# Optimization experiments

Hardware: AMD Instinct MI355X
Metric: run time of the kernel (lower is better)

## Reference

```python
import jax, jax.numpy as jnp
import numpy as np

D, NH, B, N, P = 512, 4, 4096, 30, 30  # embed_dim, num_heads, batch, seq, num_positional_embeddings


def _ln(x, g, b, eps=1e-5):
    mu = jnp.mean(x, axis=-1, keepdims=True)
    var = jnp.mean((x - mu) ** 2, axis=-1, keepdims=True)
    return g * (x - mu) / jnp.sqrt(var + eps) + b


def setup_inputs() -> dict:
    key = jax.random.key(0)
    ks = jax.random.split(key, 8)
    s = 0.02
    x = jax.random.normal(ks[0], (B, N, D), jnp.float32)
    attention_mask = jnp.zeros((B, N), dtype=bool)
    order = jax.random.randint(ks[1], (B, N), 0, P)
    num_docs = jnp.full((B,), float(N), jnp.float32)
    docs_weights = jax.random.uniform(ks[2], (B, N), jnp.float32)
    clusters_centroids = jax.random.normal(ks[3], (B, D), jnp.float32)
    pos_emb = (jax.random.normal(ks[4], (P + 1, D), jnp.float32) * s).at[P].set(0.0)
    fc1_w1 = jax.random.normal(ks[5], (2 * D + 1, D), jnp.float32) * s
    fc1_b1 = jnp.zeros((D,), jnp.float32)
    fc1_w2 = jax.random.normal(ks[6], (D, NH), jnp.float32) * s
    fc1_b2 = jnp.zeros((NH,), jnp.float32)
    fc2_w = jax.random.normal(ks[7], (NH * D, D), jnp.float32) * s
    fc2_b = jnp.zeros((D,), jnp.float32)
    return dict(
        x=x, attention_mask=attention_mask, order=order, num_docs=num_docs,
        docs_weights=docs_weights, clusters_centroids=clusters_centroids,
        pos_emb=pos_emb, fc1_w1=fc1_w1, fc1_b1=fc1_b1, fc1_w2=fc1_w2, fc1_b2=fc1_b2,
        fc2_w=fc2_w, fc2_b=fc2_b,
        ln1_g=jnp.ones((D,), jnp.float32), ln1_b=jnp.zeros((D,), jnp.float32),
        ln2_g=jnp.ones((NH * D,), jnp.float32), ln2_b=jnp.zeros((NH * D,), jnp.float32),
        ln3_g=jnp.ones((D,), jnp.float32), ln3_b=jnp.zeros((D,), jnp.float32),
        ln4_g=jnp.ones((D,), jnp.float32), ln4_b=jnp.zeros((D,), jnp.float32),
    )


def reference(x, attention_mask, order, num_docs, docs_weights, clusters_centroids,
              pos_emb, fc1_w1, fc1_b1, fc1_w2, fc1_b2, fc2_w, fc2_b,
              ln1_g, ln1_b, ln2_g, ln2_b, ln3_g, ln3_b, ln4_g, ln4_b):
    eps = 1e-8
    # norm_1: F.normalize(x, dim=2, eps=1e-8)
    xn = x / jnp.maximum(jnp.linalg.norm(x, axis=2, keepdims=True), eps)
    # input layernorm
    x1 = _ln(xn, ln1_g, ln1_b)
    xp = x1 + pos_emb[order]  # [B,N,D]
    # weighted mean pool of x_positions
    mp = jnp.sum(xp * docs_weights[:, :, None], axis=1, keepdims=True) / num_docs[:, None, None]  # [B,1,D]
    # cosine similarity between mean_pool and each token (torch eps=1e-8)
    num = jnp.sum(mp * xp, axis=2)  # [B,N]
    den = jnp.maximum(jnp.linalg.norm(mp, axis=2) * jnp.linalg.norm(xp, axis=2), eps)
    cos = (num / den)[:, :, None]  # [B,N,1]
    fc1_in = jnp.concatenate([xp, jnp.broadcast_to(mp, xp.shape), cos], axis=2)  # [B,N,2D+1]
    Z = jnp.tanh(fc1_in @ fc1_w1 + fc1_b1) @ fc1_w2 + fc1_b2  # [B,N,H]
    Z = jnp.where(attention_mask[:, :, None], -jnp.inf, Z)
    A = jax.nn.softmax(Z, axis=1)  # [B,N,H]
    b, n, h = A.shape
    d = x1.shape[2]
    # Faithful to the original reshape([B*H, N, 1]) on a [B,N,H]-contiguous tensor
    A_h = A.reshape(b, h, n)
    Hh = jnp.einsum('bhn,bnd->bhd', A_h, x1).reshape(b, h * d)  # [B, H*D]
    # residual: weighted mean pool of x (post ln1), tiled per head
    mpx = jnp.sum(x1 * docs_weights[:, :, None], axis=1) / num_docs[:, None]  # [B,D]
    Hh = _ln(Hh + jnp.tile(mpx, (1, h)), ln2_g, ln2_b)
    pred = _ln(Hh @ fc2_w + fc2_b, ln3_g, ln3_b)  # afterFC layernorm
    pred = _ln(pred + jnp.mean(Hh.reshape(b, h, d), axis=1), ln4_g, ln4_b)
    return pred
```

## Files before the change

### kernel.cpp

```cpp
#include <hip/hip_runtime.h>
#include <hip/hip_bf16.h>

#define B_ 4096
#define N_ 30
#define D_ 512
#define H_ 4
#define M_ (B_*N_)
#define PE_ROWS 31

typedef unsigned short u16;
typedef __attribute__((ext_vector_type(8))) short bf16x8;
typedef __attribute__((ext_vector_type(4))) float f32x4;

__device__ __forceinline__ float bf2f(u16 s) { return __uint_as_float(((unsigned)s) << 16); }
__device__ __forceinline__ u16 f2bf(float f) {
  __hip_bfloat16 h = __float2bfloat16(f);
  return *reinterpret_cast<u16*>(&h);
}

__device__ __forceinline__ float ftanh(float x) {
  float e = __expf(2.f * x);
  return 1.f - 2.f * __builtin_amdgcn_rcpf(e + 1.f);
}

__device__ __forceinline__ void gll16(const void* g, void* l) {
  __builtin_amdgcn_global_load_lds(
      (const __attribute__((address_space(1))) unsigned int*)g,
      (__attribute__((address_space(3))) unsigned int*)l, 16, 0, 0);
}

__device__ __forceinline__ float wsum(float v) {
  #pragma unroll
  for (int m = 32; m >= 1; m >>= 1) v += __shfl_xor(v, m);
  return v;
}
__device__ __forceinline__ float wmax(float v) {
  #pragma unroll
  for (int m = 32; m >= 1; m >>= 1) v = fmaxf(v, __shfl_xor(v, m));
  return v;
}

__global__ __launch_bounds__(512) void k1_prep(
    const float* __restrict__ x, const int* __restrict__ order,
    const float* __restrict__ ndocs, const float* __restrict__ dw,
    const float* __restrict__ pe, const float* __restrict__ g1,
    const float* __restrict__ bln1,
    u16* __restrict__ x1bf, u16* __restrict__ mpbf, float* __restrict__ mpx,
    float* __restrict__ cosb) {
  __shared__ float lds_mp[8*512];
  __shared__ float lds_mpx[8*512];
  __shared__ float xps[32];
  int b = blockIdx.x;
  int tid = threadIdx.x;
  int wid = tid >> 6, lane = tid & 63;
  int d0 = lane * 8;
  float g[8], bl[8];
  *(float4*)&g[0]  = *(const float4*)&g1[d0];
  *(float4*)&g[4]  = *(const float4*)&g1[d0+4];
  *(float4*)&bl[0] = *(const float4*)&bln1[d0];
  *(float4*)&bl[4] = *(const float4*)&bln1[d0+4];
  float xp_reg[4][8];
  float accmp[8] = {0,0,0,0,0,0,0,0}, accmpx[8] = {0,0,0,0,0,0,0,0};
  #pragma unroll
  for (int t = 0; t < 4; ++t) {
    int n = wid + 8*t;
    if (n < N_) {
      int tok = b*N_ + n;
      float v[8];
      *(float4*)&v[0] = *(const float4*)&x[(size_t)tok*D_ + d0];
      *(float4*)&v[4] = *(const float4*)&x[(size_t)tok*D_ + d0 + 4];
      float ss = 0.f, sm = 0.f;
      #pragma unroll
      for (int i = 0; i < 8; ++i) { ss += v[i]*v[i]; sm += v[i]; }
      ss = wsum(ss); sm = wsum(sm);
      float inv = 1.f / fmaxf(sqrtf(ss), 1e-8f);
      float mu = sm * inv * (1.f/D_);
      float m2 = ss*inv*inv*(1.f/D_);
      float rs = 1.f / sqrtf(m2 - mu*mu + 1e-5f);
      int o = order[tok];
      float p8[8];
      *(float4*)&p8[0] = *(const float4*)&pe[(size_t)o*D_ + d0];
      *(float4*)&p8[4] = *(const float4*)&pe[(size_t)o*D_ + d0 + 4];
      float wv = dw[tok];
      float sq = 0.f;
      bf16x8 xb;
      #pragma unroll
      for (int i = 0; i < 8; ++i) {
        float x1v = g[i]*((v[i]*inv - mu)*rs) + bl[i];
        xb[i] = (short)f2bf(x1v);
        float xpv = x1v + p8[i];
        xp_reg[t][i] = xpv;
        accmp[i]  += wv*xpv;
        accmpx[i] += wv*x1v;
        sq += xpv*xpv;
      }
      *(bf16x8*)&x1bf[(size_t)tok*D_ + d0] = xb;
      sq = wsum(sq);
      if (lane == 0) xps[n] = sq;
    }
  }
  #pragma unroll
  for (int i = 0; i < 8; i += 4) {
    *(float4*)&lds_mp[wid*512 + d0 + i]  = *(float4*)&accmp[i];
    *(float4*)&lds_mpx[wid*512 + d0 + i] = *(float4*)&accmpx[i];
  }
  __syncthreads();
  float invnd = 1.f / ndocs[b];
  float mpv[8] = {0,0,0,0,0,0,0,0}, mpxv[8] = {0,0,0,0,0,0,0,0};
  #pragma unroll
  for (int w = 0; w < 8; ++w) {
    #pragma unroll
    for (int i = 0; i < 8; i += 4) {
      float4 a = *(float4*)&lds_mp[w*512 + d0 + i];
      mpv[i+0] += a.x; mpv[i+1] += a.y; mpv[i+2] += a.z; mpv[i+3] += a.w;
      float4 c = *(float4*)&lds_mpx[w*512 + d0 + i];
      mpxv[i+0] += c.x; mpxv[i+1] += c.y; mpxv[i+2] += c.z; mpxv[i+3] += c.w;
    }
  }
  #pragma unroll
  for (int i = 0; i < 8; ++i) { mpv[i] *= invnd; mpxv[i] *= invnd; }
  if (wid == 0) {
    bf16x8 mb;
    #pragma unroll
    for (int i = 0; i < 8; ++i) mb[i] = (short)f2bf(mpv[i]);
    *(bf16x8*)&mpbf[(size_t)b*D_ + d0] = mb;
  }
  if (wid == 1) {
    #pragma unroll
    for (int i = 0; i < 8; i += 4)
      *(float4*)&mpx[(size_t)b*D_ + d0 + i] = *(float4*)&mpxv[i];
  }
  float mn = 0.f;
  #pragma unroll
  for (int i = 0; i < 8; ++i) mn += mpv[i]*mpv[i];
  float mpn = sqrtf(wsum(mn));
  #pragma unroll
  for (int t = 0; t < 4; ++t) {
    int n = wid + 8*t;
    if (n < N_) {
      float dot = 0.f;
      #pragma unroll
      for (int i = 0; i < 8; ++i) dot += mpv[i]*xp_reg[t][i];
      dot = wsum(dot);
      if (lane == 0)
        cosb[b*N_ + n] = dot / fmaxf(mpn * sqrtf(xps[n]), 1e-8f);
    }
  }
}

__global__ __launch_bounds__(512) void k_pew(
    const float* __restrict__ pe, const float* __restrict__ w1,
    float* __restrict__ peW) {
  int p = blockIdx.x, j = threadIdx.x;
  float acc = 0.f;
  for (int dd = 0; dd < D_; ++dd) acc += pe[p*D_ + dd] * w1[(size_t)dd*D_ + j];
  peW[p*D_ + j] = acc;
}

__global__ __launch_bounds__(256) void k_tcvt(
    const float* __restrict__ in, u16* __restrict__ out, int Kdim, int Jdim) {
  __shared__ float tile[64][65];
  int k0 = blockIdx.x * 64, j0 = blockIdx.y * 64;
  int t = threadIdx.x;
  int tr = t >> 4, tc4 = (t & 15) * 4;
  #pragma unroll
  for (int i = 0; i < 4; ++i) {
    int k = k0 + tr + i*16;
    float4 v = *(const float4*)&in[(size_t)k*Jdim + j0 + tc4];
    tile[tr + i*16][tc4+0] = v.x;
    tile[tr + i*16][tc4+1] = v.y;
    tile[tr + i*16][tc4+2] = v.z;
    tile[tr + i*16][tc4+3] = v.w;
  }
  __syncthreads();
  #pragma unroll
  for (int i = 0; i < 4; ++i) {
    int j = tr + i*16;
    uint2 u;
    u.x = (unsigned)f2bf(tile[tc4+0][j]) | ((unsigned)f2bf(tile[tc4+1][j]) << 16);
    u.y = (unsigned)f2bf(tile[tc4+2][j]) | ((unsigned)f2bf(tile[tc4+3][j]) << 16);
    *(uint2*)&out[(size_t)(j0+j)*Kdim + k0 + tc4] = u;
  }
}

__global__ __launch_bounds__(256, 3) void k2_mpw(
    const u16* __restrict__ mpbf, const u16* __restrict__ w1mT,
    const float* __restrict__ b1, float* __restrict__ mpW) {
  __shared__ __align__(16) u16 As[128*64];
  __shared__ __align__(16) u16 Bs[128*64];
  int tid = threadIdx.x;
  int lane = tid & 63, wid = tid >> 6;
  int wg = (blockIdx.x & 7)*16 + (blockIdx.x >> 3);
  int colb = wg & 3, rowb = wg >> 2;
  int row0 = rowb*128, col0 = colb*128;
  int wm = wid >> 1, wn = wid & 1;
  int lr = lane & 15, lk = lane >> 4;
  int srow = lane >> 3;
  int skel = ((lane & 7) ^ srow) << 3;
  f32x4 acc[4][4];
  #pragma unroll
  for (int nf = 0; nf < 4; ++nf) {
    float bv = b1[col0 + wn*64 + nf*16 + lr];
    #pragma unroll
    for (int mf = 0; mf < 4; ++mf)
      acc[mf][nf] = (f32x4){bv, bv, bv, bv};
  }
  for (int k0 = 0; k0 < D_; k0 += 64) {
    __syncthreads();
    #pragma unroll
    for (int i = 0; i < 4; ++i) {
      int rb = wid*32 + i*8;
      gll16(&mpbf[(size_t)(row0 + rb + srow)*D_ + k0 + skel], &As[rb*64]);
      gll16(&w1mT[(size_t)(col0 + rb + srow)*D_ + k0 + skel], &Bs[rb*64]);
    }
    __syncthreads();
    #pragma unroll
    for (int kk = 0; kk < 2; ++kk) {
      int kb = (kk*64 + lk*16) ^ ((lr & 7) << 4);
      bf16x8 a[4];
      #pragma unroll
      for (int mf = 0; mf < 4; ++mf)
        a[mf] = *(const bf16x8*)((const char*)As + (wm*64 + mf*16 + lr)*128 + kb);
      #pragma unroll
      for (int nf = 0; nf < 4; ++nf) {
        bf16x8 bfr = *(const bf16x8*)((const char*)Bs + (wn*64 + nf*16 + lr)*128 + kb);
        #pragma unroll
        for (int mf = 0; mf < 4; ++mf)
          acc[mf][nf] = __builtin_amdgcn_mfma_f32_16x16x32_bf16(a[mf], bfr, acc[mf][nf], 0, 0, 0);
      }
    }
  }
  #pragma unroll
  for (int mf = 0; mf < 4; ++mf)
    #pragma unroll
    for (int nf = 0; nf < 4; ++nf)
      #pragma unroll
      for (int r = 0; r < 4; ++r) {
        int m = row0 + wm*64 + mf*16 + lk*4 + r;
        int j = col0 + wn*64 + nf*16 + lr;
        mpW[(size_t)m*D_ + j] = acc[mf][nf][r];
      }
}

__global__ __launch_bounds__(256, 3) void k4_fc1(
    const u16* __restrict__ x1bf, const u16* __restrict__ w1T,
    const float* __restrict__ w1, const float* __restrict__ w2,
    const int* __restrict__ order, const float* __restrict__ cosb,
    const float* __restrict__ mpW, const float* __restrict__ peW,
    float* __restrict__ Zp) {
  __shared__ __align__(16) u16 As[128*64];
  __shared__ __align__(16) u16 Bs[128*64];
  __shared__ float zred[2*128*4];
  int tid = threadIdx.x;
  int lane = tid & 63, wid = tid >> 6;
  int col0 = blockIdx.x * 128;
  int row0 = blockIdx.y * 128;
  int wm = wid >> 1, wn = wid & 1;
  int lr = lane & 15, lk = lane >> 4;
  int srow = lane >> 3;
  int skel = ((lane & 7) ^ srow) << 3;
  float wl[4];
  #pragma unroll
  for (int nf = 0; nf < 4; ++nf)
    wl[nf] = w1[(size_t)1024*D_ + col0 + wn*64 + nf*16 + lr];
  f32x4 acc[4][4];
  #pragma unroll
  for (int mf = 0; mf < 4; ++mf) {
    #pragma unroll
    for (int r = 0; r < 4; ++r) {
      int m = row0 + wm*64 + mf*16 + lk*4 + r;
      int bidx = m / N_;
      int o = order[m];
      float cs = cosb[m];
      #pragma unroll
      for (int nf = 0; nf < 4; ++nf) {
        int jl = col0 + wn*64 + nf*16 + lr;
        acc[mf][nf][r] = mpW[(size_t)bidx*D_ + jl] + peW[o*D_ + jl] + cs*wl[nf];
      }
    }
  }
  for (int k0 = 0; k0 < D_; k0 += 64) {
    __syncthreads();
    #pragma unroll
    for (int i = 0; i < 4; ++i) {
      int rb = wid*32 + i*8;
      gll16(&x1bf[(size_t)(row0 + rb + srow)*D_ + k0 + skel], &As[rb*64]);
      gll16(&w1T [(size_t)(col0 + rb + srow)*D_ + k0 + skel], &Bs[rb*64]);
    }
    __syncthreads();
    #pragma unroll
    for (int kk = 0; kk < 2; ++kk) {
      int kb = (kk*64 + lk*16) ^ ((lr & 7) << 4);
      bf16x8 a[4];
      #pragma unroll
      for (int mf = 0; mf < 4; ++mf)
        a[mf] = *(const bf16x8*)((const char*)As + (wm*64 + mf*16 + lr)*128 + kb);
      #pragma unroll
      for (int nf = 0; nf < 4; ++nf) {
        bf16x8 bfr = *(const bf16x8*)((const char*)Bs + (wn*64 + nf*16 + lr)*128 + kb);
        #pragma unroll
        for (int mf = 0; mf < 4; ++mf)
          acc[mf][nf] = __builtin_amdgcn_mfma_f32_16x16x32_bf16(a[mf], bfr, acc[mf][nf], 0, 0, 0);
      }
    }
  }
  float w2r[4][4];
  #pragma unroll
  for (int nf = 0; nf < 4; ++nf)
    *(float4*)w2r[nf] = *(const float4*)&w2[(col0 + wn*64 + nf*16 + lr)*4];
  #pragma unroll
  for (int mf = 0; mf < 4; ++mf) {
    #pragma unroll
    for (int r = 0; r < 4; ++r) {
      int rowt = wm*64 + mf*16 + lk*4 + r;
      float z0=0.f, z1=0.f, z2=0.f, z3=0.f;
      #pragma unroll
      for (int nf = 0; nf < 4; ++nf) {
        float t = ftanh(acc[mf][nf][r]);
        z0 += t * w2r[nf][0]; z1 += t * w2r[nf][1];
        z2 += t * w2r[nf][2]; z3 += t * w2r[nf][3];
      }
      #pragma unroll
      for (int msk = 1; msk <= 8; msk <<= 1) {
        z0 += __shfl_xor(z0, msk); z1 += __shfl_xor(z1, msk);
        z2 += __shfl_xor(z2, msk); z3 += __shfl_xor(z3, msk);
      }
      if (lr == 0)
        *(float4*)&zred[(wn*128 + rowt)*4] = make_float4(z0, z1, z2, z3);
    }
  }
  __syncthreads();
  if (tid < 128) {
    float4 s0 = *(float4*)&zred[tid*4];
    float4 s1 = *(float4*)&zred[(128 + tid)*4];
    *(float4*)&Zp[((size_t)blockIdx.x*M_ + row0 + tid)*4] =
        make_float4(s0.x+s1.x, s0.y+s1.y, s0.z+s1.z, s0.w+s1.w);
  }
}

__global__ __launch_bounds__(512) void k5_attn(
    const float* __restrict__ Zp, const float* __restrict__ b2,
    const unsigned char* __restrict__ amask, const u16* __restrict__ x1bf,
    const float* __restrict__ mpx, const float* __restrict__ g2,
    const float* __restrict__ bln2, u16* __restrict__ Hh2bf,
    float* __restrict__ hmean) {
  __shared__ float abuf[8][120];
  int tid = threadIdx.x;
  int wid = tid >> 6, lane = tid & 63;
  int b = blockIdx.x*8 + wid;
  bool act = lane < N_;
  int tok = b*N_ + (act ? lane : 0);
  float zz[4] = {-INFINITY, -INFINITY, -INFINITY, -INFINITY};
  if (act) {
    float4 za = *(const float4*)&Zp[(size_t)tok*4];
    float4 zb = *(const float4*)&Zp[((size_t)M_ + tok)*4];
    float4 zc = *(const float4*)&Zp[((size_t)2*M_ + tok)*4];
    float4 zd = *(const float4*)&Zp[((size_t)3*M_ + tok)*4];
    float4 bv = *(const float4*)b2;
    zz[0] = za.x+zb.x+zc.x+zd.x+bv.x; zz[1] = za.y+zb.y+zc.y+zd.y+bv.y;
    zz[2] = za.z+zb.z+zc.z+zd.z+bv.z; zz[3] = za.w+zb.w+zc.w+zd.w+bv.w;
    if (amask[tok]) { zz[0]=zz[1]=zz[2]=zz[3]=-INFINITY; }
  }
  float p[4];
  #pragma unroll
  for (int h = 0; h < 4; ++h) {
    float mx = wmax(zz[h]);
    float e = act ? __expf(zz[h] - mx) : 0.f;
    float s = wsum(e);
    p[h] = e / s;
  }
  if (act) *(float4*)&abuf[wid][lane*4] = make_float4(p[0], p[1], p[2], p[3]);
  __syncthreads();
  float hv[4][8] = {};
  const u16* xr = &x1bf[(size_t)b*N_*D_ + lane*8];
  for (int j = 0; j < N_; ++j) {
    bf16x8 xb = *(const bf16x8*)(xr + (size_t)j*D_);
    float xv[8];
    #pragma unroll
    for (int e = 0; e < 8; ++e) xv[e] = bf2f((u16)xb[e]);
    #pragma unroll
    for (int i = 0; i < 4; ++i) {
      float a = abuf[wid][i*N_ + j];
      #pragma unroll
      for (int e = 0; e < 8; ++e) hv[i][e] += a * xv[e];
    }
  }
  float mpxv[8];
  *(float4*)&mpxv[0] = *(const float4*)&mpx[(size_t)b*D_ + lane*8];
  *(float4*)&mpxv[4] = *(const float4*)&mpx[(size_t)b*D_ + lane*8 + 4];
  float s1 = 0.f, s2 = 0.f;
  #pragma unroll
  for (int i = 0; i < 4; ++i)
    #pragma unroll
    for (int e = 0; e < 8; ++e) {
      hv[i][e] += mpxv[e];
      s1 += hv[i][e];
      s2 += hv[i][e]*hv[i][e];
    }
  s1 = wsum(s1); s2 = wsum(s2);
  float mu = s1 * (1.f/2048.f);
  float var = s2 * (1.f/2048.f) - mu*mu;
  float rs = 1.f / sqrtf(var + 1e-5f);
  float hm[8] = {0,0,0,0,0,0,0,0};
  #pragma unroll
  for (int i = 0; i < 4; ++i) {
    int idx = i*D_ + lane*8;
    float gg[8], bb[8];
    *(float4*)&gg[0] = *(const float4*)&g2[idx];
    *(float4*)&gg[4] = *(const float4*)&g2[idx+4];
    *(float4*)&bb[0] = *(const float4*)&bln2[idx];
    *(float4*)&bb[4] = *(const float4*)&bln2[idx+4];
    bf16x8 ob;
    #pragma unroll
    for (int e = 0; e < 8; ++e) {
      float v = gg[e]*((hv[i][e]-mu)*rs) + bb[e];
      hm[e] += v;
      ob[e] = (short)f2bf(v);
    }
    *(bf16x8*)&Hh2bf[(size_t)b*2048 + idx] = ob;
  }
  #pragma unroll
  for (int e = 0; e < 8; ++e) hm[e] *= 0.25f;
  *(float4*)&hmean[(size_t)b*D_ + lane*8]     = *(float4*)&hm[0];
  *(float4*)&hmean[(size_t)b*D_ + lane*8 + 4] = *(float4*)&hm[4];
}

__global__ __launch_bounds__(256, 3) void k6_fc2(
    const u16* __restrict__ Hh2bf, const u16* __restrict__ fwT,
    float* __restrict__ pred_p) {
  __shared__ __align__(16) u16 As[128*64];
  __shared__ __align__(16) u16 Bs[128*64];
  int tid = threadIdx.x;
  int lane = tid & 63, wid = tid >> 6;
  int wg = (blockIdx.x & 7)*64 + (blockIdx.x >> 3);
  int kz = wg >> 7;
  int rem = wg & 127;
  int rowb = rem >> 2, colb = rem & 3;
  int row0 = rowb*128, col0 = colb*128;
  int kbase = kz*512;
  int wm = wid >> 1, wn = wid & 1;
  int lr = lane & 15, lk = lane >> 4;
  int srow = lane >> 3;
  int skel = ((lane & 7) ^ srow) << 3;
  f32x4 acc[4][4] = {};
  for (int k0 = kbase; k0 < kbase + 512; k0 += 64) {
    __syncthreads();
    #pragma unroll
    for (int i = 0; i < 4; ++i) {
      int rb = wid*32 + i*8;
      gll16(&Hh2bf[(size_t)(row0 + rb + srow)*2048 + k0 + skel], &As[rb*64]);
      gll16(&fwT  [(size_t)(col0 + rb + srow)*2048 + k0 + skel], &Bs[rb*64]);
    }
    __syncthreads();
    #pragma unroll
    for (int kk = 0; kk < 2; ++kk) {
      int kb = (kk*64 + lk*16) ^ ((lr & 7) << 4);
      bf16x8 a[4];
      #pragma unroll
      for (int mf = 0; mf < 4; ++mf)
        a[mf] = *(const bf16x8*)((const char*)As + (wm*64 + mf*16 + lr)*128 + kb);
      #pragma unroll
      for (int nf = 0; nf < 4; ++nf) {
        bf16x8 bfr = *(const bf16x8*)((const char*)Bs + (wn*64 + nf*16 + lr)*128 + kb);
        #pragma unroll
        for (int mf = 0; mf < 4; ++mf)
          acc[mf][nf] = __builtin_amdgcn_mfma_f32_16x16x32_bf16(a[mf], bfr, acc[mf][nf], 0, 0, 0);
      }
    }
  }
  float* dst = pred_p + (size_t)kz * B_ * D_;
  #pragma unroll
  for (int mf = 0; mf < 4; ++mf)
    #pragma unroll
    for (int nf = 0; nf < 4; ++nf)
      #pragma unroll
      for (int r = 0; r < 4; ++r) {
        int m = row0 + wm*64 + mf*16 + lk*4 + r;
        int j = col0 + wn*64 + nf*16 + lr;
        dst[(size_t)m*D_ + j] = acc[mf][nf][r];
      }
}

__global__ __launch_bounds__(512) void k7_final(
    const float* __restrict__ pred_p, const float* __restrict__ hmean,
    const float* __restrict__ fb,
    const float* __restrict__ g3, const float* __restrict__ b3,
    const float* __restrict__ g4, const float* __restrict__ b4,
    float* __restrict__ out) {
  int tid = threadIdx.x;
  int wid = tid >> 6, lane = tid & 63;
  int b = blockIdx.x*8 + wid;
  int d0 = lane*8;
  size_t i = (size_t)b*D_ + d0;
  size_t BD = (size_t)B_*D_;
  float p[8];
  #pragma unroll
  for (int e = 0; e < 8; e += 4) {
    float4 a0 = *(const float4*)&pred_p[i+e];
    float4 a1 = *(const float4*)&pred_p[BD+i+e];
    float4 a2 = *(const float4*)&pred_p[2*BD+i+e];
    float4 a3 = *(const float4*)&pred_p[3*BD+i+e];
    float4 fv = *(const float4*)&fb[d0+e];
    p[e+0] = a0.x+a1.x+a2.x+a3.x+fv.x;
    p[e+1] = a0.y+a1.y+a2.y+a3.y+fv.y;
    p[e+2] = a0.z+a1.z+a2.z+a3.z+fv.z;
    p[e+3] = a0.w+a1.w+a2.w+a3.w+fv.w;
  }
  float s1 = 0.f, s2 = 0.f;
  #pragma unroll
  for (int e = 0; e < 8; ++e) { s1 += p[e]; s2 += p[e]*p[e]; }
  s1 = wsum(s1); s2 = wsum(s2);
  float mu = s1*(1.f/D_);
  float var = s2*(1.f/D_) - mu*mu;
  float rs = 1.f / sqrtf(var + 1e-5f);
  float g3v[8], b3v[8], hmv[8], q[8];
  *(float4*)&g3v[0] = *(const float4*)&g3[d0];
  *(float4*)&g3v[4] = *(const float4*)&g3[d0+4];
  *(float4*)&b3v[0] = *(const float4*)&b3[d0];
  *(float4*)&b3v[4] = *(const float4*)&b3[d0+4];
  *(float4*)&hmv[0] = *(const float4*)&hmean[i];
  *(float4*)&hmv[4] = *(const float4*)&hmean[i+4];
  float t1 = 0.f, t2 = 0.f;
  #pragma unroll
  for (int e = 0; e < 8; ++e) {
    q[e] = g3v[e]*((p[e]-mu)*rs) + b3v[e] + hmv[e];
    t1 += q[e]; t2 += q[e]*q[e];
  }
  t1 = wsum(t1); t2 = wsum(t2);
  mu = t1*(1.f/D_);
  var = t2*(1.f/D_) - mu*mu;
  rs = 1.f / sqrtf(var + 1e-5f);
  float g4v[8], b4v[8], o[8];
  *(float4*)&g4v[0] = *(const float4*)&g4[d0];
  *(float4*)&g4v[4] = *(const float4*)&g4[d0+4];
  *(float4*)&b4v[0] = *(const float4*)&b4[d0];
  *(float4*)&b4v[4] = *(const float4*)&b4[d0+4];
  #pragma unroll
  for (int e = 0; e < 8; ++e) o[e] = g4v[e]*((q[e]-mu)*rs) + b4v[e];
  *(float4*)&out[i]   = *(float4*)&o[0];
  *(float4*)&out[i+4] = *(float4*)&o[4];
}

extern "C" void kernel_launch(void* const* d_in, const int* in_sizes, int n_in,
                              void* d_out, int out_size, void* d_ws, size_t ws_size,
                              hipStream_t stream) {
  const float* x      = (const float*)d_in[0];
  const unsigned char* amask = (const unsigned char*)d_in[1];
  const int*   order  = (const int*)d_in[2];
  const float* ndocs  = (const float*)d_in[3];
  const float* dw     = (const float*)d_in[4];
  const float* pe     = (const float*)d_in[6];
  const float* w1     = (const float*)d_in[7];
  const float* b1     = (const float*)d_in[8];
  const float* w2     = (const float*)d_in[9];
  const float* b2     = (const float*)d_in[10];
  const float* fw     = (const float*)d_in[11];
  const float* fb     = (const float*)d_in[12];
  const float* g1     = (const float*)d_in[13];
  const float* bln1   = (const float*)d_in[14];
  const float* g2     = (const float*)d_in[15];
  const float* bln2   = (const float*)d_in[16];
  const float* g3     = (const float*)d_in[17];
  const float* b3     = (const float*)d_in[18];
  const float* g4     = (const float*)d_in[19];
  const float* b4     = (const float*)d_in[20];
  float* out = (float*)d_out;

  char* ws = (char*)d_ws;
  size_t off = 0;
  u16*   x1bf   = (u16*)(ws + off);   off += (size_t)M_*D_*2;
  u16*   mpbf   = (u16*)(ws + off);   off += (size_t)B_*D_*2;
  float* mpx    = (float*)(ws + off); off += (size_t)B_*D_*4;
  float* mpW    = (float*)(ws + off); off += (size_t)B_*D_*4;
  float* hmean  = (float*)(ws + off); off += (size_t)B_*D_*4;
  float* peW    = (float*)(ws + off); off += (size_t)PE_ROWS*D_*4;
  float* cosb   = (float*)(ws + off); off += (size_t)M_*4;
  float* Zp     = (float*)(ws + off); off += (size_t)4*M_*4*4;
  float* pred_p = (float*)(ws + off); off += (size_t)4*B_*D_*4;
  u16*   Hh2bf  = (u16*)(ws + off);   off += (size_t)B_*2048*2;
  u16*   w1T    = (u16*)(ws + off);   off += (size_t)D_*D_*2;
  u16*   w1mT   = (u16*)(ws + off);   off += (size_t)D_*D_*2;
  u16*   fwT    = (u16*)(ws + off);   off += (size_t)D_*2048*2;
  (void)ws_size; (void)in_sizes; (void)n_in; (void)out_size;

  k_tcvt<<<dim3(8, 8), 256, 0, stream>>>(w1, w1T, 512, 512);
  k_tcvt<<<dim3(8, 8), 256, 0, stream>>>(w1 + 512*512, w1mT, 512, 512);
  k_tcvt<<<dim3(32, 8), 256, 0, stream>>>(fw, fwT, 2048, 512);
  k_pew<<<PE_ROWS, 512, 0, stream>>>(pe, w1, peW);
  k1_prep<<<B_, 512, 0, stream>>>(x, order, ndocs, dw, pe, g1, bln1,
                                  x1bf, mpbf, mpx, cosb);
  k2_mpw<<<128, 256, 0, stream>>>(mpbf, w1mT, b1, mpW);
  k4_fc1<<<dim3(4, M_/128), 256, 0, stream>>>(x1bf, w1T, w1, w2, order, cosb,
                                              mpW, peW, Zp);
  k5_attn<<<B_/8, 512, 0, stream>>>(Zp, b2, amask, x1bf, mpx, g2, bln2,
                                    Hh2bf, hmean);
  k6_fc2<<<512, 256, 0, stream>>>(Hh2bf, fwT, pred_p);
  k7_final<<<B_/8, 512, 0, stream>>>(pred_p, hmean, fb, g3, b3, g4, b4, out);
}
```

Baseline: 325.9 us.

## Enlarge fc1 GEMM tiles to 256x256 with double-buffered LDS and block swizzle

The fc1 kernel moves from 128x128 tiles with 256 threads to 256x256 tiles with 512 threads. Each wave now holds an 8x4 grid of MFMA accumulators. Global-to-LDS loads are double-buffered so the next K slice is fetched while the current one is computed, which leaves one barrier per iteration. Block indices are swizzled, and the Z partial sums now come from two column blocks instead of four, so the attention kernel reads half as many partials. The cost is a large LDS footprint (128 KB, so likely one block per CU) and heavy register pressure, which risks spills or low occupancy.

```diff
diff --git a/kernel.cpp b/kernel.cpp
--- a/kernel.cpp
+++ b/kernel.cpp
@@ -242,20 +242,19 @@
       }
 }
 
-__global__ __launch_bounds__(256, 3) void k4_fc1(
+__global__ __launch_bounds__(512, 2) void k4_fc1(
     const u16* __restrict__ x1bf, const u16* __restrict__ w1T,
     const float* __restrict__ w1, const float* __restrict__ w2,
     const int* __restrict__ order, const float* __restrict__ cosb,
     const float* __restrict__ mpW, const float* __restrict__ peW,
     float* __restrict__ Zp) {
-  __shared__ __align__(16) u16 As[128*64];
-  __shared__ __align__(16) u16 Bs[128*64];
-  __shared__ float zred[2*128*4];
+  __shared__ __align__(16) u16 buf[2][2*256*64];
   int tid = threadIdx.x;
   int lane = tid & 63, wid = tid >> 6;
-  int col0 = blockIdx.x * 128;
-  int row0 = blockIdx.y * 128;
-  int wm = wid >> 1, wn = wid & 1;
+  int wg = (blockIdx.x & 7)*120 + (blockIdx.x >> 3);
+  int colb = wg & 1, rowb = wg >> 1;
+  int col0 = colb*256, row0 = rowb*256;
+  int wm = wid >> 2, wn = wid & 3;
   int lr = lane & 15, lk = lane >> 4;
   int srow = lane >> 3;
   int skel = ((lane & 7) ^ srow) << 3;
@@ -263,12 +262,12 @@
   #pragma unroll
   for (int nf = 0; nf < 4; ++nf)
     wl[nf] = w1[(size_t)1024*D_ + col0 + wn*64 + nf*16 + lr];
-  f32x4 acc[4][4];
-  #pragma unroll
-  for (int mf = 0; mf < 4; ++mf) {
+  f32x4 acc[8][4];
+  #pragma unroll
+  for (int mf = 0; mf < 8; ++mf) {
     #pragma unroll
     for (int r = 0; r < 4; ++r) {
-      int m = row0 + wm*64 + mf*16 + lk*4 + r;
+      int m = row0 + wm*128 + mf*16 + lk*4 + r;
       int bidx = m / N_;
       int o = order[m];
       float cs = cosb[m];
@@ -279,40 +278,55 @@
       }
     }
   }
-  for (int k0 = 0; k0 < D_; k0 += 64) {
-    __syncthreads();
-    #pragma unroll
-    for (int i = 0; i < 4; ++i) {
-      int rb = wid*32 + i*8;
-      gll16(&x1bf[(size_t)(row0 + rb + srow)*D_ + k0 + skel], &As[rb*64]);
-      gll16(&w1T [(size_t)(col0 + rb + srow)*D_ + k0 + skel], &Bs[rb*64]);
-    }
-    __syncthreads();
+  float w2r[4][4];
+  #pragma unroll
+  for (int nf = 0; nf < 4; ++nf)
+    *(float4*)w2r[nf] = *(const float4*)&w2[(col0 + wn*64 + nf*16 + lr)*4];
+
+#define K4_STAGE(c, k0)                                                     \
+  {                                                                         \
+    u16* Ad = &buf[c][0];                                                   \
+    u16* Bd = &buf[c][16384];                                               \
+    _Pragma("unroll")                                                       \
+    for (int i = 0; i < 4; ++i) {                                           \
+      int rb = wid*32 + i*8;                                                \
+      gll16(&x1bf[(size_t)(row0 + rb + srow)*D_ + (k0) + skel], &Ad[rb*64]);\
+      gll16(&w1T [(size_t)(col0 + rb + srow)*D_ + (k0) + skel], &Bd[rb*64]);\
+    }                                                                       \
+  }
+
+  K4_STAGE(0, 0);
+  __syncthreads();
+  int cur = 0;
+  for (int t = 0; t < 8; ++t) {
+    if (t < 7) K4_STAGE(cur^1, (t+1)*64);
+    const u16* A = &buf[cur][0];
+    const u16* Bx = &buf[cur][16384];
     #pragma unroll
     for (int kk = 0; kk < 2; ++kk) {
       int kb = (kk*64 + lk*16) ^ ((lr & 7) << 4);
-      bf16x8 a[4];
-      #pragma unroll
-      for (int mf = 0; mf < 4; ++mf)
-        a[mf] = *(const bf16x8*)((const char*)As + (wm*64 + mf*16 + lr)*128 + kb);
+      bf16x8 a[8];
+      #pragma unroll
+      for (int mf = 0; mf < 8; ++mf)
+        a[mf] = *(const bf16x8*)((const char*)A + (wm*128 + mf*16 + lr)*128 + kb);
       #pragma unroll
       for (int nf = 0; nf < 4; ++nf) {
-        bf16x8 bfr = *(const bf16x8*)((const char*)Bs + (wn*64 + nf*16 + lr)*128 + kb);
+        bf16x8 bfr = *(const bf16x8*)((const char*)Bx + (wn*64 + nf*16 + lr)*128 + kb);
         #pragma unroll
-        for (int mf = 0; mf < 4; ++mf)
+        for (int mf = 0; mf < 8; ++mf)
           acc[mf][nf] = __builtin_amdgcn_mfma_f32_16x16x32_bf16(a[mf], bfr, acc[mf][nf], 0, 0, 0);
       }
     }
-  }
-  float w2r[4][4];
-  #pragma unroll
-  for (int nf = 0; nf < 4; ++nf)
-    *(float4*)w2r[nf] = *(const float4*)&w2[(col0 + wn*64 + nf*16 + lr)*4];
-  #pragma unroll
-  for (int mf = 0; mf < 4; ++mf) {
+    __syncthreads();
+    cur ^= 1;
+  }
+#undef K4_STAGE
+  float* zred = (float*)buf;
+  #pragma unroll
+  for (int mf = 0; mf < 8; ++mf) {
     #pragma unroll
     for (int r = 0; r < 4; ++r) {
-      int rowt = wm*64 + mf*16 + lk*4 + r;
+      int rowt = wm*128 + mf*16 + lk*4 + r;
       float z0=0.f, z1=0.f, z2=0.f, z3=0.f;
       #pragma unroll
       for (int nf = 0; nf < 4; ++nf) {
@@ -326,15 +340,18 @@
         z2 += __shfl_xor(z2, msk); z3 += __shfl_xor(z3, msk);
       }
       if (lr == 0)
-        *(float4*)&zred[(wn*128 + rowt)*4] = make_float4(z0, z1, z2, z3);
+        *(float4*)&zred[(wn*256 + rowt)*4] = make_float4(z0, z1, z2, z3);
     }
   }
   __syncthreads();
-  if (tid < 128) {
+  if (tid < 256) {
     float4 s0 = *(float4*)&zred[tid*4];
-    float4 s1 = *(float4*)&zred[(128 + tid)*4];
-    *(float4*)&Zp[((size_t)blockIdx.x*M_ + row0 + tid)*4] =
-        make_float4(s0.x+s1.x, s0.y+s1.y, s0.z+s1.z, s0.w+s1.w);
+    float4 s1 = *(float4*)&zred[(256 + tid)*4];
+    float4 s2 = *(float4*)&zred[(512 + tid)*4];
+    float4 s3 = *(float4*)&zred[(768 + tid)*4];
+    *(float4*)&Zp[((size_t)colb*M_ + row0 + tid)*4] =
+        make_float4(s0.x+s1.x+s2.x+s3.x, s0.y+s1.y+s2.y+s3.y,
+                    s0.z+s1.z+s2.z+s3.z, s0.w+s1.w+s2.w+s3.w);
   }
 }
 
@@ -354,11 +371,9 @@
   if (act) {
     float4 za = *(const float4*)&Zp[(size_t)tok*4];
     float4 zb = *(const float4*)&Zp[((size_t)M_ + tok)*4];
-    float4 zc = *(const float4*)&Zp[((size_t)2*M_ + tok)*4];
-    float4 zd = *(const float4*)&Zp[((size_t)3*M_ + tok)*4];
     float4 bv = *(const float4*)b2;
-    zz[0] = za.x+zb.x+zc.x+zd.x+bv.x; zz[1] = za.y+zb.y+zc.y+zd.y+bv.y;
-    zz[2] = za.z+zb.z+zc.z+zd.z+bv.z; zz[3] = za.w+zb.w+zc.w+zd.w+bv.w;
+    zz[0] = za.x+zb.x+bv.x; zz[1] = za.y+zb.y+bv.y;
+    zz[2] = za.z+zb.z+bv.z; zz[3] = za.w+zb.w+bv.w;
     if (amask[tok]) { zz[0]=zz[1]=zz[2]=zz[3]=-INFINITY; }
   }
   float p[4];
@@ -575,7 +590,7 @@
   float* hmean  = (float*)(ws + off); off += (size_t)B_*D_*4;
   float* peW    = (float*)(ws + off); off += (size_t)PE_ROWS*D_*4;
   float* cosb   = (float*)(ws + off); off += (size_t)M_*4;
-  float* Zp     = (float*)(ws + off); off += (size_t)4*M_*4*4;
+  float* Zp     = (float*)(ws + off); off += (size_t)2*M_*4*4;
   float* pred_p = (float*)(ws + off); off += (size_t)4*B_*D_*4;
   u16*   Hh2bf  = (u16*)(ws + off);   off += (size_t)B_*2048*2;
   u16*   w1T    = (u16*)(ws + off);   off += (size_t)D_*D_*2;
@@ -590,8 +605,8 @@
   k1_prep<<<B_, 512, 0, stream>>>(x, order, ndocs, dw, pe, g1, bln1,
                                   x1bf, mpbf, mpx, cosb);
   k2_mpw<<<128, 256, 0, stream>>>(mpbf, w1mT, b1, mpW);
-  k4_fc1<<<dim3(4, M_/128), 256, 0, stream>>>(x1bf, w1T, w1, w2, order, cosb,
-                                              mpW, peW, Zp);
+  k4_fc1<<<960, 512, 0, stream>>>(x1bf, w1T, w1, w2, order, cosb,
+                                  mpW, peW, Zp);
   k5_attn<<<B_/8, 512, 0, stream>>>(Zp, b2, amask, x1bf, mpx, g2, bln2,
                                     Hh2bf, hmean);
   k6_fc2<<<512, 256, 0, stream>>>(Hh2bf, fwT, pred_p);
```

Result: slower. 403.3 us (+23.8%).

## Compute full 512-wide fc1 row tile per block, dropping partial Z buffers

Applied to the files above, without the earlier changes.

The fc1 kernel now uses 512-thread blocks that each cover 128 rows across all 512 output columns, so the A tile is loaded once rather than four times and the tanh·w2 reduction completes inside the block. Z is written directly, with no four-way partial buffer for the attention kernel to sum. Block indices are swizzled across 8 groups, and zred reuses the As shared memory. In exchange, each thread keeps twice the accumulators (128 floats), which raises register pressure, and the Bs tile grows to 64KB, which limits occupancy.

```diff
diff --git a/kernel.cpp b/kernel.cpp
--- a/kernel.cpp
+++ b/kernel.cpp
@@ -242,28 +242,27 @@
       }
 }
 
-__global__ __launch_bounds__(256, 3) void k4_fc1(
+__global__ __launch_bounds__(512, 2) void k4_fc1(
     const u16* __restrict__ x1bf, const u16* __restrict__ w1T,
     const float* __restrict__ w1, const float* __restrict__ w2,
     const int* __restrict__ order, const float* __restrict__ cosb,
     const float* __restrict__ mpW, const float* __restrict__ peW,
-    float* __restrict__ Zp) {
+    float* __restrict__ Z) {
   __shared__ __align__(16) u16 As[128*64];
-  __shared__ __align__(16) u16 Bs[128*64];
-  __shared__ float zred[2*128*4];
+  __shared__ __align__(16) u16 Bs[512*64];
   int tid = threadIdx.x;
   int lane = tid & 63, wid = tid >> 6;
-  int col0 = blockIdx.x * 128;
-  int row0 = blockIdx.y * 128;
-  int wm = wid >> 1, wn = wid & 1;
+  int wg = (blockIdx.x & 7)*120 + (blockIdx.x >> 3);
+  int row0 = wg * 128;
+  int wm = wid >> 2, wn = wid & 3;
   int lr = lane & 15, lk = lane >> 4;
   int srow = lane >> 3;
   int skel = ((lane & 7) ^ srow) << 3;
-  float wl[4];
-  #pragma unroll
-  for (int nf = 0; nf < 4; ++nf)
-    wl[nf] = w1[(size_t)1024*D_ + col0 + wn*64 + nf*16 + lr];
-  f32x4 acc[4][4];
+  float wl[8];
+  #pragma unroll
+  for (int nf = 0; nf < 8; ++nf)
+    wl[nf] = w1[(size_t)1024*D_ + wn*128 + nf*16 + lr];
+  f32x4 acc[4][8];
   #pragma unroll
   for (int mf = 0; mf < 4; ++mf) {
     #pragma unroll
@@ -273,8 +272,8 @@
       int o = order[m];
       float cs = cosb[m];
       #pragma unroll
-      for (int nf = 0; nf < 4; ++nf) {
-        int jl = col0 + wn*64 + nf*16 + lr;
+      for (int nf = 0; nf < 8; ++nf) {
+        int jl = wn*128 + nf*16 + lr;
         acc[mf][nf][r] = mpW[(size_t)bidx*D_ + jl] + peW[o*D_ + jl] + cs*wl[nf];
       }
     }
@@ -282,10 +281,14 @@
   for (int k0 = 0; k0 < D_; k0 += 64) {
     __syncthreads();
     #pragma unroll
-    for (int i = 0; i < 4; ++i) {
-      int rb = wid*32 + i*8;
+    for (int i = 0; i < 2; ++i) {
+      int rb = wid*16 + i*8;
       gll16(&x1bf[(size_t)(row0 + rb + srow)*D_ + k0 + skel], &As[rb*64]);
-      gll16(&w1T [(size_t)(col0 + rb + srow)*D_ + k0 + skel], &Bs[rb*64]);
+    }
+    #pragma unroll
+    for (int i = 0; i < 8; ++i) {
+      int rb = wid*64 + i*8;
+      gll16(&w1T[(size_t)(rb + srow)*D_ + k0 + skel], &Bs[rb*64]);
     }
     __syncthreads();
     #pragma unroll
@@ -296,18 +299,20 @@
       for (int mf = 0; mf < 4; ++mf)
         a[mf] = *(const bf16x8*)((const char*)As + (wm*64 + mf*16 + lr)*128 + kb);
       #pragma unroll
-      for (int nf = 0; nf < 4; ++nf) {
-        bf16x8 bfr = *(const bf16x8*)((const char*)Bs + (wn*64 + nf*16 + lr)*128 + kb);
+      for (int nf = 0; nf < 8; ++nf) {
+        bf16x8 bfr = *(const bf16x8*)((const char*)Bs + (wn*128 + nf*16 + lr)*128 + kb);
         #pragma unroll
         for (int mf = 0; mf < 4; ++mf)
           acc[mf][nf] = __builtin_amdgcn_mfma_f32_16x16x32_bf16(a[mf], bfr, acc[mf][nf], 0, 0, 0);
       }
     }
   }
-  float w2r[4][4];
-  #pragma unroll
-  for (int nf = 0; nf < 4; ++nf)
-    *(float4*)w2r[nf] = *(const float4*)&w2[(col0 + wn*64 + nf*16 + lr)*4];
+  float w2r[8][4];
+  #pragma unroll
+  for (int nf = 0; nf < 8; ++nf)
+    *(float4*)w2r[nf] = *(const float4*)&w2[(wn*128 + nf*16 + lr)*4];
+  __syncthreads();
+  float* zred = (float*)As;
   #pragma unroll
   for (int mf = 0; mf < 4; ++mf) {
     #pragma unroll
@@ -315,7 +320,7 @@
       int rowt = wm*64 + mf*16 + lk*4 + r;
       float z0=0.f, z1=0.f, z2=0.f, z3=0.f;
       #pragma unroll
-      for (int nf = 0; nf < 4; ++nf) {
+      for (int nf = 0; nf < 8; ++nf) {
         float t = ftanh(acc[mf][nf][r]);
         z0 += t * w2r[nf][0]; z1 += t * w2r[nf][1];
         z2 += t * w2r[nf][2]; z3 += t * w2r[nf][3];
@@ -333,13 +338,16 @@
   if (tid < 128) {
     float4 s0 = *(float4*)&zred[tid*4];
     float4 s1 = *(float4*)&zred[(128 + tid)*4];
-    *(float4*)&Zp[((size_t)blockIdx.x*M_ + row0 + tid)*4] =
-        make_float4(s0.x+s1.x, s0.y+s1.y, s0.z+s1.z, s0.w+s1.w);
+    float4 s2 = *(float4*)&zred[(256 + tid)*4];
+    float4 s3 = *(float4*)&zred[(384 + tid)*4];
+    *(float4*)&Z[(size_t)(row0 + tid)*4] =
+        make_float4(s0.x+s1.x+s2.x+s3.x, s0.y+s1.y+s2.y+s3.y,
+                    s0.z+s1.z+s2.z+s3.z, s0.w+s1.w+s2.w+s3.w);
   }
 }
 
 __global__ __launch_bounds__(512) void k5_attn(
-    const float* __restrict__ Zp, const float* __restrict__ b2,
+    const float* __restrict__ Z, const float* __restrict__ b2,
     const unsigned char* __restrict__ amask, const u16* __restrict__ x1bf,
     const float* __restrict__ mpx, const float* __restrict__ g2,
     const float* __restrict__ bln2, u16* __restrict__ Hh2bf,
@@ -352,13 +360,10 @@
   int tok = b*N_ + (act ? lane : 0);
   float zz[4] = {-INFINITY, -INFINITY, -INFINITY, -INFINITY};
   if (act) {
-    float4 za = *(const float4*)&Zp[(size_t)tok*4];
-    float4 zb = *(const float4*)&Zp[((size_t)M_ + tok)*4];
-    float4 zc = *(const float4*)&Zp[((size_t)2*M_ + tok)*4];
-    float4 zd = *(const float4*)&Zp[((size_t)3*M_ + tok)*4];
+    float4 za = *(const float4*)&Z[(size_t)tok*4];
     float4 bv = *(const float4*)b2;
-    zz[0] = za.x+zb.x+zc.x+zd.x+bv.x; zz[1] = za.y+zb.y+zc.y+zd.y+bv.y;
-    zz[2] = za.z+zb.z+zc.z+zd.z+bv.z; zz[3] = za.w+zb.w+zc.w+zd.w+bv.w;
+    zz[0] = za.x+bv.x; zz[1] = za.y+bv.y;
+    zz[2] = za.z+bv.z; zz[3] = za.w+bv.w;
     if (amask[tok]) { zz[0]=zz[1]=zz[2]=zz[3]=-INFINITY; }
   }
   float p[4];
@@ -575,7 +580,7 @@
   float* hmean  = (float*)(ws + off); off += (size_t)B_*D_*4;
   float* peW    = (float*)(ws + off); off += (size_t)PE_ROWS*D_*4;
   float* cosb   = (float*)(ws + off); off += (size_t)M_*4;
-  float* Zp     = (float*)(ws + off); off += (size_t)4*M_*4*4;
+  float* Z      = (float*)(ws + off); off += (size_t)M_*4*4;
   float* pred_p = (float*)(ws + off); off += (size_t)4*B_*D_*4;
   u16*   Hh2bf  = (u16*)(ws + off);   off += (size_t)B_*2048*2;
   u16*   w1T    = (u16*)(ws + off);   off += (size_t)D_*D_*2;
@@ -590,9 +595,9 @@
   k1_prep<<<B_, 512, 0, stream>>>(x, order, ndocs, dw, pe, g1, bln1,
                                   x1bf, mpbf, mpx, cosb);
   k2_mpw<<<128, 256, 0, stream>>>(mpbf, w1mT, b1, mpW);
-  k4_fc1<<<dim3(4, M_/128), 256, 0, stream>>>(x1bf, w1T, w1, w2, order, cosb,
-                                              mpW, peW, Zp);
-  k5_attn<<<B_/8, 512, 0, stream>>>(Zp, b2, amask, x1bf, mpx, g2, bln2,
+  k4_fc1<<<960, 512, 0, stream>>>(x1bf, w1T, w1, w2, order, cosb,
+                                  mpW, peW, Z);
+  k5_attn<<<B_/8, 512, 0, stream>>>(Z, b2, amask, x1bf, mpx, g2, bln2,
                                     Hh2bf, hmean);
   k6_fc2<<<512, 256, 0, stream>>>(Hh2bf, fwT, pred_p);
   k7_final<<<B_/8, 512, 0, stream>>>(pred_p, hmean, fb, g3, b3, g4, b4, out);
```

Result: slower. 344.8 us (+5.8%).
